# Performance work log

Hardware: AMD Instinct MI355X
Metric: run time of the kernel (lower is better)

The kernel has to match this reference:

```python
import jax, jax.numpy as jnp
import numpy as np

PATCH = 16  # patch_size

def _patchify(images, p=PATCH):
    # images: [B, H, W] -> patches: [B, N, p*p] in raster order
    B, H, W = images.shape
    x = images.reshape(B, H // p, p, W // p, p)
    x = x.transpose(0, 1, 3, 2, 4)  # [B, H/p, W/p, p, p]
    return x.reshape(B, (H // p) * (W // p), p * p)

def setup_inputs() -> dict:
    key = jax.random.key(0)
    k1, k2 = jax.random.split(key)
    images = jax.random.normal(k1, (64, 256, 256), dtype=jnp.float32)
    vocab = jax.random.normal(k2, (4096, 256), dtype=jnp.float32)  # [V, patch^2]
    return {"images": images, "vocab": vocab}

def reference(images, vocab):
    # forward_patches: patchify (raster ordering -> identity permutation)
    patches = _patchify(images)  # [B, N, D]
    # forward_tokens: torch.cdist + argmin. argmin of Euclidean distance
    # equals argmin of squared distance; expand ||x-v||^2 to avoid the
    # explicit [B, N, V, D] difference tensor.
    v2 = jnp.sum(vocab * vocab, axis=-1)                      # [V]
    xv = jnp.einsum('bnd,vd->bnv', patches, vocab)            # [B, N, V]
    x2 = jnp.sum(patches * patches, axis=-1, keepdims=True)   # [B, N, 1]
    d2 = x2 - 2.0 * xv + v2                                   # [B, N, V]
    tokens = jnp.argmin(d2, axis=-1)                          # [B, N] int
    return patches, tokens
```

## Files before the change

### kernel.cpp

```cpp
#include <hip/hip_runtime.h>
#include <math.h>

#define PS      16
#define D       256
#define V       4096
#define M       16384
#define NSPLIT  64
#define PAIR_CAP 1048576
#define QMARGIN 130

typedef _Float16 half8 __attribute__((ext_vector_type(8)));
typedef _Float16 half4 __attribute__((ext_vector_type(4)));
typedef float    f32x4 __attribute__((ext_vector_type(4)));

__device__ __forceinline__ void gload_lds16(const void* g, void* l) {
  __builtin_amdgcn_global_load_lds(
      (const __attribute__((address_space(1))) unsigned int*)g,
      (__attribute__((address_space(3))) unsigned int*)l, 16, 0, 0);
}


__global__ __launch_bounds__(256) void prep_kernel(
    const float* __restrict__ img, const float* __restrict__ vocab,
    float* __restrict__ outp, _Float16* __restrict__ Ah2,
    _Float16* __restrict__ Vh2, float* __restrict__ v2,
    int* __restrict__ paircount) {
  if (blockIdx.x < 4096) {
    if (blockIdx.x == 0 && threadIdx.x == 0) *paircount = 0;
    const int t  = blockIdx.x * 256 + threadIdx.x;
    const int o4 = t << 2;
    const int m   = o4 >> 8;
    const int d   = o4 & 255;
    const int b   = m >> 8;
    const int n   = m & 255;
    const int py = n >> 4, px = n & 15, i = d >> 4, j = d & 15;
    const float4 v = *(const float4*)(img + (b << 16) + ((py * PS + i) << 8) + px * PS + j);
    *(float4*)(outp + o4) = v;
    half4 h = { (_Float16)v.x, (_Float16)v.y, (_Float16)v.z, (_Float16)v.w };
    const int fa = (m >> 6) * 16384 + (d >> 5) * 2048 + ((m >> 4) & 3) * 512 +
                   ((d >> 3) & 3) * 128 + (m & 15) * 8 + (d & 7);
    *(half4*)(Ah2 + fa) = h;
  } else {
    const int gtid = (blockIdx.x - 4096) * 256 + threadIdx.x;
    const int c    = gtid >> 6;
    const int lane = gtid & 63;
    const int d0   = lane << 2;
    const float4 v = *(const float4*)(vocab + (size_t)c * D + d0);
    half4 h = { (_Float16)v.x, (_Float16)v.y, (_Float16)v.z, (_Float16)v.w };
    const int fv = (c >> 8) * 65536 + (d0 >> 5) * 8192 + ((c >> 4) & 15) * 512 +
                   ((d0 >> 3) & 3) * 128 + (c & 15) * 8 + (d0 & 7);
    *(half4*)(Vh2 + fv) = h;
    float s = v.x * v.x + v.y * v.y + v.z * v.z + v.w * v.w;
    #pragma unroll
    for (int off = 32; off > 0; off >>= 1) s += __shfl_down(s, off);
    if (lane == 0) v2[c] = s;
  }
}

__global__ __launch_bounds__(256, 5) void gemm_score_kernel(
    const _Float16* __restrict__ Ah2,
    const _Float16* __restrict__ Vh2,
    const float* __restrict__ v2,
    unsigned* __restrict__ pk1, unsigned* __restrict__ pk2) {
  __shared__ __align__(16) _Float16 Af[8 * 64 * 32];

  const int tid  = threadIdx.x;
  const int lane = tid & 63;
  const int wid  = tid >> 6;
  const int sp     = blockIdx.x;
  const int rowblk = blockIdx.y;
  const int row0 = rowblk * 64;
  const int c0w  = sp * 128 + wid * 32;

  {
    const _Float16* src = Ah2 + (size_t)rowblk * 16384 + wid * 4096 + lane * 8;
    _Float16* dst = Af + wid * 4096;
    #pragma unroll
    for (int t = 0; t < 8; ++t)
      gload_lds16(src + t * 512, dst + t * 512);
  }
  __syncthreads();

  const int cl = lane & 15;
  const int q  = lane >> 4;
  const _Float16* Ak = Af + q * 128 + cl * 8;
  const _Float16* Bk = Vh2 + (c0w >> 8) * 65536 + ((c0w >> 4) & 15) * 512 +
                       q * 128 + cl * 8;

  f32x4 acc[2][4];
  #pragma unroll
  for (int i = 0; i < 2; ++i)
    #pragma unroll
    for (int j = 0; j < 4; ++j) acc[i][j] = (f32x4){0.f, 0.f, 0.f, 0.f};

  #pragma unroll 1
  for (int kt = 0; kt < 8; ++kt) {
    half8 av[2], bp[4];
    #pragma unroll
    for (int i = 0; i < 2; ++i) av[i] = *(const half8*)(Bk + i * 512);
    #pragma unroll
    for (int j = 0; j < 4; ++j) bp[j] = *(const half8*)(Ak + j * 512);
    Bk += 8192; Ak += 2048;
    #pragma unroll
    for (int i = 0; i < 2; ++i)
      #pragma unroll
      for (int j = 0; j < 4; ++j)
        acc[i][j] = __builtin_amdgcn_mfma_f32_16x16x32_f16(av[i], bp[j], acc[i][j], 0, 0, 0);
  }

  float Cv[8];
  #pragma unroll
  for (int i = 0; i < 2; ++i) {
    const float4 vq = *(const float4*)(v2 + c0w + i * 16 + q * 4);
    #pragma unroll
    for (int r = 0; r < 4; ++r) Cv[i * 4 + r] = fmaf(vq[r], 512.0f, 524288.0f);
  }
  unsigned wk1[4], wk2[4];
  #pragma unroll
  for (int j = 0; j < 4; ++j) {
    unsigned K1 = 0xFFFFFFFFu, K2 = 0xFFFFFFFFu;
    #pragma unroll
    for (int i = 0; i < 2; ++i)
      #pragma unroll
      for (int r = 0; r < 4; ++r) {
        const unsigned key =
            ((unsigned)fmaf(-1024.0f, acc[i][j][r], Cv[i * 4 + r]) << 12) |
            (unsigned)(c0w + i * 16 + q * 4 + r);
        K2 = min(K2, max(K1, key));
        K1 = min(K1, key);
      }
    #pragma unroll
    for (int mask = 16; mask <= 32; mask <<= 1) {
      const unsigned o1 = (unsigned)__shfl_xor((int)K1, mask);
      const unsigned o2 = (unsigned)__shfl_xor((int)K2, mask);
      K2 = min(min(K2, o2), max(K1, o1));
      K1 = min(K1, o1);
    }
    wk1[j] = K1; wk2[j] = K2;
  }
  __syncthreads();
  unsigned* scr = (unsigned*)Af;
  if (q == 0) {
    #pragma unroll
    for (int j = 0; j < 4; ++j) {
      const int idx = (wid >> 1) * 256 + (wid & 1) * 128 + (j * 16 + cl) * 2;
      scr[idx] = wk1[j]; scr[idx + 1] = wk2[j];
    }
  }
  __syncthreads();
  if (tid < 128) {
    const int pair = tid >> 6, row = tid & 63;
    const unsigned a1 = scr[pair * 256 + row * 2], a2 = scr[pair * 256 + row * 2 + 1];
    const unsigned b1 = scr[pair * 256 + 128 + row * 2], b2 = scr[pair * 256 + 128 + row * 2 + 1];
    const unsigned K2 = min(min(a2, b2), max(a1, b1));
    const unsigned K1 = min(a1, b1);
    const int grp = sp * 2 + pair;
    pk1[(size_t)grp * M + row0 + row] = K1;
    pk2[(size_t)grp * M + row0 + row] = K2;
  }
}

__global__ __launch_bounds__(256) void reduce_gather_kernel(
    const unsigned* __restrict__ pk1, const unsigned* __restrict__ pk2,
    float* __restrict__ tok, unsigned long long* __restrict__ minkey,
    unsigned* __restrict__ pairs, int* __restrict__ paircount) {
  __shared__ unsigned r1[4][64], r2[4][64];
  const int tid = threadIdx.x;
  const int mo  = tid & 63;
  const int wid = tid >> 6;
  const int m = blockIdx.x * 64 + mo;
  unsigned K1 = 0xFFFFFFFFu, K2 = 0xFFFFFFFFu;
  for (int s = wid * 16; s < wid * 16 + 16; ++s) {
    const unsigned b1 = pk1[(size_t)s * M + m];
    const unsigned b2 = pk2[(size_t)s * M + m];
    K2 = min(min(K2, b2), max(K1, b1));
    K1 = min(K1, b1);
  }
  r1[wid][mo] = K1; r2[wid][mo] = K2;
  __syncthreads();
  if (tid < 64) {
    K1 = 0xFFFFFFFFu; K2 = 0xFFFFFFFFu;
    #pragma unroll
    for (int w = 0; w < 4; ++w) {
      const unsigned b1 = r1[w][mo], b2 = r2[w][mo];
      K2 = min(min(K2, b2), max(K1, b1));
      K1 = min(K1, b1);
    }
    tok[m] = (float)(K1 & 4095u);
    minkey[m] = 0xFFFFFFFFFFFFFFFFull;
    if ((int)(K2 >> 12) - (int)(K1 >> 12) <= QMARGIN) {
      const int th = (int)(K1 >> 12) + QMARGIN;
      int cnt = 0;
      for (int s = 0; s < NSPLIT; ++s) {
        const unsigned b1 = pk1[(size_t)s * M + m];
        const unsigned b2 = pk2[(size_t)s * M + m];
        cnt += ((int)(b2 >> 12) <= th) ? 64
             : (((int)(b1 >> 12) <= th) ? 1 : 0);
      }
      int base = atomicAdd(paircount, cnt);
      if (base + cnt <= PAIR_CAP) {
        const unsigned mh = (unsigned)m << 12;
        for (int s = 0; s < NSPLIT; ++s) {
          const unsigned b1 = pk1[(size_t)s * M + m];
          const unsigned b2 = pk2[(size_t)s * M + m];
          if ((int)(b2 >> 12) <= th) {
            for (int r = 0; r < 64; ++r) pairs[base + r] = mh | (unsigned)(s * 64 + r);
            base += 64;
          } else if ((int)(b1 >> 12) <= th) {
            pairs[base++] = mh | (b1 & 4095u);
          }
        }
      }
    }
  }
}

__global__ __launch_bounds__(256) void refine_score(
    const float* __restrict__ patches, const float* __restrict__ vocab,
    const unsigned* __restrict__ pairs, const int* __restrict__ paircount,
    unsigned long long* __restrict__ minkey) {
  const int lane = threadIdx.x & 63;
  const int gw = (blockIdx.x * 256 + threadIdx.x) >> 6;
  const int nw = (gridDim.x * 256) >> 6;
  int np = *paircount;
  if (np > PAIR_CAP) np = PAIR_CAP;
  for (int i = gw; i < np; i += nw) {
    const unsigned pr = pairs[i];
    const int m = pr >> 12, row = pr & 4095;
    const float4 pv = *(const float4*)(patches + (size_t)m * D + (lane << 2));
    const float4 vv = *(const float4*)(vocab + (size_t)row * D + (lane << 2));
    double acc = 0.0, df;
    df = (double)pv.x - (double)vv.x; acc = fma(df, df, acc);
    df = (double)pv.y - (double)vv.y; acc = fma(df, df, acc);
    df = (double)pv.z - (double)vv.z; acc = fma(df, df, acc);
    df = (double)pv.w - (double)vv.w; acc = fma(df, df, acc);
    #pragma unroll
    for (int off = 32; off > 0; off >>= 1) acc += __shfl_down(acc, off);
    if (lane == 0) {
      const unsigned long long key =
          ((unsigned long long)__double_as_longlong(acc) & ~0xFFFull) | (unsigned)row;
      atomicMin(&minkey[m], key);
    }
  }
}

__global__ __launch_bounds__(256) void refine_final(
    const unsigned* __restrict__ pairs, const int* __restrict__ paircount,
    const unsigned long long* __restrict__ minkey, float* __restrict__ tok) {
  int np = *paircount;
  if (np > PAIR_CAP) np = PAIR_CAP;
  for (int i = blockIdx.x * 256 + threadIdx.x; i < np; i += gridDim.x * 256) {
    const int m = pairs[i] >> 12;
    tok[m] = (float)(unsigned)(minkey[m] & 4095ull);
  }
}

extern "C" void kernel_launch(void* const* d_in, const int* in_sizes, int n_in,
                              void* d_out, int out_size, void* d_ws, size_t ws_size,
                              hipStream_t stream) {
  const float* images = (const float*)d_in[0];
  const float* vocab  = (const float*)d_in[1];
  float* out     = (float*)d_out;
  float* patches = out;
  float* tokens  = out + (size_t)M * D;

  char* ws = (char*)d_ws;
  _Float16* Ah2      = (_Float16*)(ws);
  _Float16* Vh2      = (_Float16*)(ws + 8388608);
  float*    v2       = (float*)   (ws + 10485760);
  unsigned* pk1      = (unsigned*)(ws + 10502144);
  unsigned* pk2      = (unsigned*)(ws + 14696448);
  unsigned long long* minkey = (unsigned long long*)(ws + 18890752);
  int*      paircount= (int*)     (ws + 19021824);
  unsigned* pairs    = (unsigned*)(ws + 19021888);

  prep_kernel<<<4096 + 1024, 256, 0, stream>>>(images, vocab, patches, Ah2,
                                               Vh2, v2, paircount);
  gemm_score_kernel<<<dim3(V / 128, M / 64), 256, 0, stream>>>(Ah2, Vh2, v2, pk1, pk2);
  reduce_gather_kernel<<<M / 64, 256, 0, stream>>>(pk1, pk2, tokens, minkey,
                                                   pairs, paircount);
  refine_score<<<512, 256, 0, stream>>>(patches, vocab, pairs, paircount, minkey);
  refine_final<<<64, 256, 0, stream>>>(pairs, paircount, minkey, tokens);
}
```

Before: 158.2 us.

## Software-pipeline LDS fragment loads with MFMA and move top-2 reduction to LDS

The K loop is fully unrolled with rotating register buffers, so LDS fragment loads for later k-steps are issued while MFMAs for earlier steps run. Each MFMA group is wrapped in s_setprio to raise wave priority. The cross-lane shuffle top-2 reduction is removed: all four quad lanes write their partial keys to LDS and the final 128 threads merge eight entries each. The aim is to hide LDS latency and cut shuffle instructions, at the cost of more registers and more LDS traffic in the epilogue.

```diff
diff --git a/kernel.cpp b/kernel.cpp
--- a/kernel.cpp
+++ b/kernel.cpp
@@ -93,20 +93,42 @@
     #pragma unroll
     for (int j = 0; j < 4; ++j) acc[i][j] = (f32x4){0.f, 0.f, 0.f, 0.f};
 
-  #pragma unroll 1
-  for (int kt = 0; kt < 8; ++kt) {
-    half8 av[2], bp[4];
-    #pragma unroll
-    for (int i = 0; i < 2; ++i) av[i] = *(const half8*)(Bk + i * 512);
-    #pragma unroll
-    for (int j = 0; j < 4; ++j) bp[j] = *(const half8*)(Ak + j * 512);
-    Bk += 8192; Ak += 2048;
-    #pragma unroll
-    for (int i = 0; i < 2; ++i)
-      #pragma unroll
-      for (int j = 0; j < 4; ++j)
-        acc[i][j] = __builtin_amdgcn_mfma_f32_16x16x32_f16(av[i], bp[j], acc[i][j], 0, 0, 0);
-  }
+  half8 av[4][2], bp[2][4];
+#define LV(S, KT) do {                                              \
+    av[S][0] = *(const half8*)(Bk + (KT) * 8192);                   \
+    av[S][1] = *(const half8*)(Bk + (KT) * 8192 + 512);             \
+  } while (0)
+#define LA(S, KT) do {                                              \
+    bp[S][0] = *(const half8*)(Ak + (KT) * 2048);                   \
+    bp[S][1] = *(const half8*)(Ak + (KT) * 2048 + 512);             \
+    bp[S][2] = *(const half8*)(Ak + (KT) * 2048 + 1024);            \
+    bp[S][3] = *(const half8*)(Ak + (KT) * 2048 + 1536);            \
+  } while (0)
+#define MM(SV, SA) do {                                             \
+    __builtin_amdgcn_s_setprio(1);                                  \
+    acc[0][0] = __builtin_amdgcn_mfma_f32_16x16x32_f16(av[SV][0], bp[SA][0], acc[0][0], 0, 0, 0); \
+    acc[0][1] = __builtin_amdgcn_mfma_f32_16x16x32_f16(av[SV][0], bp[SA][1], acc[0][1], 0, 0, 0); \
+    acc[0][2] = __builtin_amdgcn_mfma_f32_16x16x32_f16(av[SV][0], bp[SA][2], acc[0][2], 0, 0, 0); \
+    acc[0][3] = __builtin_amdgcn_mfma_f32_16x16x32_f16(av[SV][0], bp[SA][3], acc[0][3], 0, 0, 0); \
+    acc[1][0] = __builtin_amdgcn_mfma_f32_16x16x32_f16(av[SV][1], bp[SA][0], acc[1][0], 0, 0, 0); \
+    acc[1][1] = __builtin_amdgcn_mfma_f32_16x16x32_f16(av[SV][1], bp[SA][1], acc[1][1], 0, 0, 0); \
+    acc[1][2] = __builtin_amdgcn_mfma_f32_16x16x32_f16(av[SV][1], bp[SA][2], acc[1][2], 0, 0, 0); \
+    acc[1][3] = __builtin_amdgcn_mfma_f32_16x16x32_f16(av[SV][1], bp[SA][3], acc[1][3], 0, 0, 0); \
+    __builtin_amdgcn_s_setprio(0);                                  \
+  } while (0)
+
+  LV(0, 0); LV(1, 1); LA(0, 0);
+  LV(2, 2); LA(1, 1); MM(0, 0);
+  LV(3, 3); LA(0, 2); MM(1, 1);
+  LV(0, 4); LA(1, 3); MM(2, 0);
+  LV(1, 5); LA(0, 4); MM(3, 1);
+  LV(2, 6); LA(1, 5); MM(0, 0);
+  LV(3, 7); LA(0, 6); MM(1, 1);
+            LA(1, 7); MM(2, 0);
+                      MM(3, 1);
+#undef LV
+#undef LA
+#undef MM
 
   float Cv[8];
   #pragma unroll
@@ -129,31 +151,29 @@
         K2 = min(K2, max(K1, key));
         K1 = min(K1, key);
       }
-    #pragma unroll
-    for (int mask = 16; mask <= 32; mask <<= 1) {
-      const unsigned o1 = (unsigned)__shfl_xor((int)K1, mask);
-      const unsigned o2 = (unsigned)__shfl_xor((int)K2, mask);
-      K2 = min(min(K2, o2), max(K1, o1));
-      K1 = min(K1, o1);
-    }
     wk1[j] = K1; wk2[j] = K2;
   }
   __syncthreads();
   unsigned* scr = (unsigned*)Af;
-  if (q == 0) {
-    #pragma unroll
-    for (int j = 0; j < 4; ++j) {
-      const int idx = (wid >> 1) * 256 + (wid & 1) * 128 + (j * 16 + cl) * 2;
-      scr[idx] = wk1[j]; scr[idx + 1] = wk2[j];
-    }
+  #pragma unroll
+  for (int j = 0; j < 4; ++j) {
+    const int idx = ((wid * 64 + j * 16 + cl) * 4 + q) * 2;
+    scr[idx] = wk1[j]; scr[idx + 1] = wk2[j];
   }
   __syncthreads();
   if (tid < 128) {
     const int pair = tid >> 6, row = tid & 63;
-    const unsigned a1 = scr[pair * 256 + row * 2], a2 = scr[pair * 256 + row * 2 + 1];
-    const unsigned b1 = scr[pair * 256 + 128 + row * 2], b2 = scr[pair * 256 + 128 + row * 2 + 1];
-    const unsigned K2 = min(min(a2, b2), max(a1, b1));
-    const unsigned K1 = min(a1, b1);
+    unsigned K1 = 0xFFFFFFFFu, K2 = 0xFFFFFFFFu;
+    #pragma unroll
+    for (int w = 0; w < 2; ++w) {
+      const unsigned* s = scr + ((pair * 2 + w) * 64 + row) * 8;
+      #pragma unroll
+      for (int qq = 0; qq < 4; ++qq) {
+        const unsigned b1 = s[qq * 2], b2 = s[qq * 2 + 1];
+        K2 = min(min(K2, b2), max(K1, b1));
+        K1 = min(K1, b1);
+      }
+    }
     const int grp = sp * 2 + pair;
     pk1[(size_t)grp * M + row0 + row] = K1;
     pk2[(size_t)grp * M + row0 + row] = K2;
```

After: 181.6 us. 14.8% more time.

## Widen GEMM blocks to 512 threads and software-pipeline vocab loads

Applied to the files above, without the earlier changes.

The score GEMM now uses 8 waves per block, each covering 256 vocab columns, so the 64-row A tile staged in LDS is shared by twice as many columns and half as many blocks reload it. The K loop is unrolled by two with double-buffered register loads of the vocab fragments, so global loads for the next step are issued before the current MFMAs. The MFMA bursts are wrapped in s_setprio to favour matrix issue. Risks include higher register pressure under the new launch bounds (512 threads, 6 blocks) and a different grid shape. The reduction writes four partial groups per block; the total number of groups written is unchanged.

```diff
diff --git a/kernel.cpp b/kernel.cpp
--- a/kernel.cpp
+++ b/kernel.cpp
@@ -57,7 +57,7 @@
   }
 }
 
-__global__ __launch_bounds__(256, 5) void gemm_score_kernel(
+__global__ __launch_bounds__(512, 6) void gemm_score_kernel(
     const _Float16* __restrict__ Ah2,
     const _Float16* __restrict__ Vh2,
     const float* __restrict__ v2,
@@ -70,13 +70,13 @@
   const int sp     = blockIdx.x;
   const int rowblk = blockIdx.y;
   const int row0 = rowblk * 64;
-  const int c0w  = sp * 128 + wid * 32;
+  const int c0w  = sp * 256 + wid * 32;
 
   {
-    const _Float16* src = Ah2 + (size_t)rowblk * 16384 + wid * 4096 + lane * 8;
-    _Float16* dst = Af + wid * 4096;
-    #pragma unroll
-    for (int t = 0; t < 8; ++t)
+    const _Float16* src = Ah2 + (size_t)rowblk * 16384 + wid * 2048 + lane * 8;
+    _Float16* dst = Af + wid * 2048;
+    #pragma unroll
+    for (int t = 0; t < 4; ++t)
       gload_lds16(src + t * 512, dst + t * 512);
   }
   __syncthreads();
@@ -84,7 +84,7 @@
   const int cl = lane & 15;
   const int q  = lane >> 4;
   const _Float16* Ak = Af + q * 128 + cl * 8;
-  const _Float16* Bk = Vh2 + (c0w >> 8) * 65536 + ((c0w >> 4) & 15) * 512 +
+  const _Float16* Bk = Vh2 + sp * 65536 + wid * 1024 +
                        q * 128 + cl * 8;
 
   f32x4 acc[2][4];
@@ -93,20 +93,49 @@
     #pragma unroll
     for (int j = 0; j < 4; ++j) acc[i][j] = (f32x4){0.f, 0.f, 0.f, 0.f};
 
+  half8 av0[2], av1[2], bp[4];
+#define LAV(B, OFF) do {                                            \
+    B[0] = *(const half8*)(Bk + (OFF));                             \
+    B[1] = *(const half8*)(Bk + (OFF) + 512);                       \
+  } while (0)
+#define LBP(OFF) do {                                               \
+    bp[0] = *(const half8*)(Ak + (OFF));                            \
+    bp[1] = *(const half8*)(Ak + (OFF) + 512);                      \
+    bp[2] = *(const half8*)(Ak + (OFF) + 1024);                     \
+    bp[3] = *(const half8*)(Ak + (OFF) + 1536);                     \
+  } while (0)
+#define MMC(AV) do {                                                \
+    __builtin_amdgcn_s_setprio(1);                                  \
+    acc[0][0] = __builtin_amdgcn_mfma_f32_16x16x32_f16(AV[0], bp[0], acc[0][0], 0, 0, 0); \
+    acc[0][1] = __builtin_amdgcn_mfma_f32_16x16x32_f16(AV[0], bp[1], acc[0][1], 0, 0, 0); \
+    acc[0][2] = __builtin_amdgcn_mfma_f32_16x16x32_f16(AV[0], bp[2], acc[0][2], 0, 0, 0); \
+    acc[0][3] = __builtin_amdgcn_mfma_f32_16x16x32_f16(AV[0], bp[3], acc[0][3], 0, 0, 0); \
+    acc[1][0] = __builtin_amdgcn_mfma_f32_16x16x32_f16(AV[1], bp[0], acc[1][0], 0, 0, 0); \
+    acc[1][1] = __builtin_amdgcn_mfma_f32_16x16x32_f16(AV[1], bp[1], acc[1][1], 0, 0, 0); \
+    acc[1][2] = __builtin_amdgcn_mfma_f32_16x16x32_f16(AV[1], bp[2], acc[1][2], 0, 0, 0); \
+    acc[1][3] = __builtin_amdgcn_mfma_f32_16x16x32_f16(AV[1], bp[3], acc[1][3], 0, 0, 0); \
+    __builtin_amdgcn_s_setprio(0);                                  \
+  } while (0)
+
+  LAV(av0, 0);
   #pragma unroll 1
-  for (int kt = 0; kt < 8; ++kt) {
-    half8 av[2], bp[4];
-    #pragma unroll
-    for (int i = 0; i < 2; ++i) av[i] = *(const half8*)(Bk + i * 512);
-    #pragma unroll
-    for (int j = 0; j < 4; ++j) bp[j] = *(const half8*)(Ak + j * 512);
-    Bk += 8192; Ak += 2048;
-    #pragma unroll
-    for (int i = 0; i < 2; ++i)
-      #pragma unroll
-      for (int j = 0; j < 4; ++j)
-        acc[i][j] = __builtin_amdgcn_mfma_f32_16x16x32_f16(av[i], bp[j], acc[i][j], 0, 0, 0);
-  }
+  for (int kt2 = 0; kt2 < 3; ++kt2) {
+    LAV(av1, 8192);
+    LBP(0);
+    MMC(av0);
+    LAV(av0, 16384);
+    LBP(2048);
+    MMC(av1);
+    Bk += 16384; Ak += 4096;
+  }
+  LAV(av1, 8192);
+  LBP(0);
+  MMC(av0);
+  LBP(2048);
+  MMC(av1);
+#undef LAV
+#undef LBP
+#undef MMC
 
   float Cv[8];
   #pragma unroll
@@ -148,13 +177,13 @@
     }
   }
   __syncthreads();
-  if (tid < 128) {
+  if (tid < 256) {
     const int pair = tid >> 6, row = tid & 63;
-    const unsigned a1 = scr[pair * 256 + row * 2], a2 = scr[pair * 256 + row * 2 + 1];
-    const unsigned b1 = scr[pair * 256 + 128 + row * 2], b2 = scr[pair * 256 + 128 + row * 2 + 1];
-    const unsigned K2 = min(min(a2, b2), max(a1, b1));
-    const unsigned K1 = min(a1, b1);
-    const int grp = sp * 2 + pair;
+    const unsigned a1k = scr[pair * 256 + row * 2], a2k = scr[pair * 256 + row * 2 + 1];
+    const unsigned b1k = scr[pair * 256 + 128 + row * 2], b2k = scr[pair * 256 + 128 + row * 2 + 1];
+    const unsigned K2 = min(min(a2k, b2k), max(a1k, b1k));
+    const unsigned K1 = min(a1k, b1k);
+    const int grp = sp * 4 + pair;
     pk1[(size_t)grp * M + row0 + row] = K1;
     pk2[(size_t)grp * M + row0 + row] = K2;
   }
@@ -276,7 +305,7 @@
 
   prep_kernel<<<4096 + 1024, 256, 0, stream>>>(images, vocab, patches, Ah2,
                                                Vh2, v2, paircount);
-  gemm_score_kernel<<<dim3(V / 128, M / 64), 256, 0, stream>>>(Ah2, Vh2, v2, pk1, pk2);
+  gemm_score_kernel<<<dim3(V / 256, M / 64), 512, 0, stream>>>(Ah2, Vh2, v2, pk1, pk2);
   reduce_gather_kernel<<<M / 64, 256, 0, stream>>>(pk1, pk2, tokens, minkey,
                                                    pairs, paircount);
   refine_score<<<512, 256, 0, stream>>>(patches, vocab, pairs, paircount, minkey);
```

Result: faster. 151.0 us (-4.5%).
